# Performance work log

Measured on AMD Instinct MI355X. Metric: run time of the kernel, lower is better.

The kernel has to match this reference:

```python
import jax, jax.numpy as jnp
import numpy as np

HIDDEN = 32
SEQ = 1440
IN = 11


def lstm_layer(x, Wih, Whh, bih, bhh):
    # x: (B, T, I); PyTorch gate order i, f, g, o stacked along first dim of W (4H, I)
    B, T, _ = x.shape
    H = Whh.shape[1]
    xg = jnp.einsum('bti,gi->btg', x, Wih) + bih + bhh  # (B, T, 4H) input projections precomputed

    def step(carry, xg_t):
        h, c = carry
        g = xg_t + h @ Whh.T  # (B, 4H)
        i, f, gg, o = jnp.split(g, 4, axis=-1)
        i = jax.nn.sigmoid(i)
        f = jax.nn.sigmoid(f)
        gg = jnp.tanh(gg)
        o = jax.nn.sigmoid(o)
        c = f * c + i * gg
        h = o * jnp.tanh(c)
        return (h, c), h

    h0 = jnp.zeros((B, H), x.dtype)
    (_, _), hs = jax.lax.scan(step, (h0, h0), jnp.swapaxes(xg, 0, 1))  # hs: (T, B, H)
    return jnp.swapaxes(hs, 0, 1)


def setup_inputs() -> dict:
    key = jax.random.key(0)
    ks = jax.random.split(key, 14)
    s = 0.1
    return {
        'x': jax.random.normal(ks[0], (1024, IN, SEQ), dtype=jnp.float32),
        'Wih0': jax.random.normal(ks[1], (4 * HIDDEN, IN), dtype=jnp.float32) * s,
        'Whh0': jax.random.normal(ks[2], (4 * HIDDEN, HIDDEN), dtype=jnp.float32) * s,
        'bih0': jax.random.normal(ks[3], (4 * HIDDEN,), dtype=jnp.float32) * s,
        'bhh0': jax.random.normal(ks[4], (4 * HIDDEN,), dtype=jnp.float32) * s,
        'Wih1': jax.random.normal(ks[5], (4 * HIDDEN, HIDDEN), dtype=jnp.float32) * s,
        'Whh1': jax.random.normal(ks[6], (4 * HIDDEN, HIDDEN), dtype=jnp.float32) * s,
        'bih1': jax.random.normal(ks[7], (4 * HIDDEN,), dtype=jnp.float32) * s,
        'bhh1': jax.random.normal(ks[8], (4 * HIDDEN,), dtype=jnp.float32) * s,
        'fc1_w': jax.random.normal(ks[9], (16, HIDDEN), dtype=jnp.float32) * s,
        'fc1_b': jax.random.normal(ks[10], (16,), dtype=jnp.float32) * s,
        'fc2_w': jax.random.normal(ks[11], (1, 16), dtype=jnp.float32) * s,
        'fc2_b': jax.random.normal(ks[12], (1,), dtype=jnp.float32) * s,
    }


def reference(x, Wih0, Whh0, bih0, bhh0, Wih1, Whh1, bih1, bhh1, fc1_w, fc1_b, fc2_w, fc2_b):
    # x.view(-1, 11, 1440).transpose(1, 2) -> (B, 1440, 11)
    xt = jnp.swapaxes(x.reshape(-1, IN, SEQ), 1, 2)
    h1 = lstm_layer(xt, Wih0, Whh0, bih0, bhh0)
    h2 = lstm_layer(h1, Wih1, Whh1, bih1, bhh1)
    out = h2[:, :SEQ - 1, :]  # out[:, -1440:-1, :] with T=1440 -> steps 0..1438
    out = jnp.tanh(out @ fc1_w.T + fc1_b)
    out = out @ fc2_w.T + fc2_b
    return out.squeeze(-1)  # (B, 1439)
```

## Files before the change

### kernel.cpp

```cpp
#include <hip/hip_runtime.h>

#define H    32
#define SEQ  1440
#define NT   (SEQ - 1)
#define INP  11
#define TC   64

#define LOG2E 1.44269504f

__device__ __forceinline__ float rcp_fast(float x)  { return __builtin_amdgcn_rcpf(x); }
__device__ __forceinline__ float exp2_fast(float x) { return __builtin_amdgcn_exp2f(x); }
__device__ __forceinline__ float tanh_f(float x) {
    return fmaf(2.f, rcp_fast(1.f + exp2_fast(x * (-2.f * LOG2E))), -1.f);
}

__global__
__attribute__((amdgpu_flat_work_group_size(128, 128)))
__attribute__((amdgpu_waves_per_eu(2, 2)))
void lstm_fused_kernel(const float* __restrict__ x,
                       const float* __restrict__ Wih0, const float* __restrict__ Whh0,
                       const float* __restrict__ bih0, const float* __restrict__ bhh0,
                       const float* __restrict__ Wih1, const float* __restrict__ Whh1,
                       const float* __restrict__ bih1, const float* __restrict__ bhh1,
                       const float* __restrict__ fc1w_g, const float* __restrict__ fc1b_g,
                       const float* __restrict__ fc2w_g, const float* __restrict__ fc2b_g,
                       float* __restrict__ out)
{
    __shared__ float h0s[2][H];
    __shared__ float h1s[2][H];
    __shared__ float xs[TC][12];
    __shared__ float h1c[TC][36];

    const int tid  = threadIdx.x;
    const int lane = tid & 63;
    const int wv   = tid >> 6;
    const int m    = lane & 15;
    const int q    = lane >> 4;
    const int jj   = wv * 16 + m;
    const int r    = q * 32 + jj;
    const int b    = blockIdx.x;

    const float gsl = ((q == 2) ? 2.f : 1.f) * LOG2E;
    const float am  = (q == 2) ? 2.f : 1.f;
    const float ab  = (q == 2) ? -1.f : 0.f;

    float wx[12];
    #pragma unroll
    for (int i = 0; i < INP; ++i) wx[i] = Wih0[r * INP + i] * gsl;
    wx[11] = 0.f;
    float wh0[H], wi1[H], wh1[H];
    #pragma unroll
    for (int k = 0; k < H; ++k) {
        wh0[k] = Whh0[r * H + k] * gsl;
        wi1[k] = Wih1[r * H + k] * gsl;
        wh1[k] = Whh1[r * H + k] * gsl;
    }
    const float bs0 = (bih0[r] + bhh0[r]) * gsl;
    const float bs1 = (bih1[r] + bhh1[r]) * gsl;

    if (tid < H) { h0s[0][tid] = 0.f; h1s[0][tid] = 0.f; }
    float c0 = 0.f, c1 = 0.f;

    const float* xb   = x   + (size_t)b * INP * SEQ;
    float*       outb = out + (size_t)b * NT;

    __syncthreads();

    for (int cbase = 0; cbase < NT; cbase += TC) {
        const int clen = min(TC, NT - cbase);

        {
            const int col = tid & 63;
            const int rw  = tid >> 6;
            #pragma unroll
            for (int ib = 0; ib < 12; ib += 2) {
                const int row = ib + rw;
                if (col < clen)
                    xs[col][row] = (row < INP) ? xb[row * SEQ + cbase + col] : 0.f;
            }
        }
        __syncthreads();

        for (int tc = 0; tc < clen; ++tc) {
            const int p = (cbase + tc) & 1;

            float act;
            {
                const float4* xv = (const float4*)xs[tc];
                const float4* hv = (const float4*)h0s[p];
                float a0 = bs0, a1 = 0.f;
                float4 x0 = xv[0], x1 = xv[1], x2 = xv[2];
                a0 = fmaf(wx[0],  x0.x, a0);  a1 = fmaf(wx[1],  x0.y, a1);
                a0 = fmaf(wx[2],  x0.z, a0);  a1 = fmaf(wx[3],  x0.w, a1);
                a0 = fmaf(wx[4],  x1.x, a0);  a1 = fmaf(wx[5],  x1.y, a1);
                a0 = fmaf(wx[6],  x1.z, a0);  a1 = fmaf(wx[7],  x1.w, a1);
                a0 = fmaf(wx[8],  x2.x, a0);  a1 = fmaf(wx[9],  x2.y, a1);
                a0 = fmaf(wx[10], x2.z, a0);
                #pragma unroll
                for (int kk = 0; kk < 4; ++kk) {
                    float4 ha = hv[kk], hb = hv[kk + 4];
                    a0 = fmaf(wh0[4*kk+0],    ha.x, a0);
                    a1 = fmaf(wh0[4*kk+1],    ha.y, a1);
                    a0 = fmaf(wh0[4*kk+2],    ha.z, a0);
                    a1 = fmaf(wh0[4*kk+3],    ha.w, a1);
                    a0 = fmaf(wh0[16+4*kk+0], hb.x, a0);
                    a1 = fmaf(wh0[16+4*kk+1], hb.y, a1);
                    a0 = fmaf(wh0[16+4*kk+2], hb.z, a0);
                    a1 = fmaf(wh0[16+4*kk+3], hb.w, a1);
                }
                float a = a0 + a1;
                act = fmaf(am, rcp_fast(1.f + exp2_fast(-a)), ab);
            }
            float gf = __shfl_xor(act, 16);
            float gg = __shfl_xor(act, 32);
            float go = __shfl_xor(act, 48);
            if (q == 0) {
                c0 = fmaf(gf, c0, act * gg);
                h0s[p ^ 1][jj] = go * tanh_f(c0);
            }
            __syncthreads();

            {
                const float4* hav = (const float4*)h0s[p ^ 1];
                const float4* hbv = (const float4*)h1s[p];
                float a0 = bs1, a1 = 0.f, a2 = 0.f, a3 = 0.f;
                #pragma unroll
                for (int kk = 0; kk < 4; ++kk) {
                    float4 ha = hav[kk], ha2 = hav[kk + 4];
                    float4 hb = hbv[kk], hb2 = hbv[kk + 4];
                    a0 = fmaf(wi1[4*kk+0],    ha.x,  a0); a1 = fmaf(wi1[4*kk+1],    ha.y,  a1);
                    a2 = fmaf(wi1[4*kk+2],    ha.z,  a2); a3 = fmaf(wi1[4*kk+3],    ha.w,  a3);
                    a0 = fmaf(wi1[16+4*kk+0], ha2.x, a0); a1 = fmaf(wi1[16+4*kk+1], ha2.y, a1);
                    a2 = fmaf(wi1[16+4*kk+2], ha2.z, a2); a3 = fmaf(wi1[16+4*kk+3], ha2.w, a3);
                    a0 = fmaf(wh1[4*kk+0],    hb.x,  a0); a1 = fmaf(wh1[4*kk+1],    hb.y,  a1);
                    a2 = fmaf(wh1[4*kk+2],    hb.z,  a2); a3 = fmaf(wh1[4*kk+3],    hb.w,  a3);
                    a0 = fmaf(wh1[16+4*kk+0], hb2.x, a0); a1 = fmaf(wh1[16+4*kk+1], hb2.y, a1);
                    a2 = fmaf(wh1[16+4*kk+2], hb2.z, a2); a3 = fmaf(wh1[16+4*kk+3], hb2.w, a3);
                }
                float a = (a0 + a1) + (a2 + a3);
                act = fmaf(am, rcp_fast(1.f + exp2_fast(-a)), ab);
            }
            gf = __shfl_xor(act, 16);
            gg = __shfl_xor(act, 32);
            go = __shfl_xor(act, 48);
            if (q == 0) {
                c1 = fmaf(gf, c1, act * gg);
                float hn = go * tanh_f(c1);
                h1s[p ^ 1][jj] = hn;
                h1c[tc][jj]    = hn;
            }
            __syncthreads();
        }

        {
            const int u = tid & 15;
            float fcw[H];
            #pragma unroll
            for (int k = 0; k < H; ++k) fcw[k] = fc1w_g[u * H + k];
            const float fcb = fc1b_g[u];
            const float f2w = fc2w_g[u];
            const float f2b = fc2b_g[0];
            #pragma unroll
            for (int rep = 0; rep < 8; ++rep) {
                const int tcl = (tid >> 4) + 8 * rep;
                if (tcl < clen) {
                    const float4* hv = (const float4*)h1c[tcl];
                    float a0 = fcb, a1 = 0.f;
                    #pragma unroll
                    for (int kk = 0; kk < 4; ++kk) {
                        float4 ha = hv[kk], hb = hv[kk + 4];
                        a0 = fmaf(fcw[4*kk+0],    ha.x, a0); a1 = fmaf(fcw[4*kk+1],    ha.y, a1);
                        a0 = fmaf(fcw[4*kk+2],    ha.z, a0); a1 = fmaf(fcw[4*kk+3],    ha.w, a1);
                        a0 = fmaf(fcw[16+4*kk+0], hb.x, a0); a1 = fmaf(fcw[16+4*kk+1], hb.y, a1);
                        a0 = fmaf(fcw[16+4*kk+2], hb.z, a0); a1 = fmaf(fcw[16+4*kk+3], hb.w, a1);
                    }
                    float yv = tanh_f(a0 + a1) * f2w;
                    yv += __shfl_xor(yv, 1);
                    yv += __shfl_xor(yv, 2);
                    yv += __shfl_xor(yv, 4);
                    yv += __shfl_xor(yv, 8);
                    if (u == 0) outb[cbase + tcl] = yv + f2b;
                }
            }
        }
        __syncthreads();
    }
}

extern "C" void kernel_launch(void* const* d_in, const int* in_sizes, int n_in,
                              void* d_out, int out_size, void* d_ws, size_t ws_size,
                              hipStream_t stream)
{
    const float* x    = (const float*)d_in[0];
    const float* Wih0 = (const float*)d_in[1];
    const float* Whh0 = (const float*)d_in[2];
    const float* bih0 = (const float*)d_in[3];
    const float* bhh0 = (const float*)d_in[4];
    const float* Wih1 = (const float*)d_in[5];
    const float* Whh1 = (const float*)d_in[6];
    const float* bih1 = (const float*)d_in[7];
    const float* bhh1 = (const float*)d_in[8];
    const float* fc1w = (const float*)d_in[9];
    const float* fc1b = (const float*)d_in[10];
    const float* fc2w = (const float*)d_in[11];
    const float* fc2b = (const float*)d_in[12];
    float* out = (float*)d_out;

    const int B = in_sizes[0] / (INP * SEQ);
    dim3 grid(B), block(128);
    hipLaunchKernelGGL(lstm_fused_kernel, grid, block, 0, stream,
                       x, Wih0, Whh0, bih0, bhh0, Wih1, Whh1, bih1, bhh1,
                       fc1w, fc1b, fc2w, fc2b, out);
}
```

Measured before the change: 1.262 ms.

## Wavefront-pipeline the two LSTM layers across separate warp halves

The block grows to 256 threads. One half runs layer 0 at step p while the other half runs layer 1 at step p-1, so each time step needs one barrier instead of two and the two layers' recurrences overlap. Each half now holds only its own layer's weights, which lowers register pressure. The FC head moves into the first iteration of the next chunk, using a double-buffered h1 cache, with a final tail pass afterwards. The cost is twice as many threads per block, which may reduce how many blocks fit per CU, plus one extra pipeline step.

After: 1.522 ms. 20.6% more time.

```diff
diff --git a/kernel.cpp b/kernel.cpp
--- a/kernel.cpp
+++ b/kernel.cpp
@@ -3,6 +3,7 @@
 #define H    32
 #define SEQ  1440
 #define NT   (SEQ - 1)
+#define NPH  SEQ
 #define INP  11
 #define TC   64
 
@@ -15,8 +16,8 @@
 }
 
 __global__
-__attribute__((amdgpu_flat_work_group_size(128, 128)))
-__attribute__((amdgpu_waves_per_eu(2, 2)))
+__attribute__((amdgpu_flat_work_group_size(256, 256)))
+__attribute__((amdgpu_waves_per_eu(2, 4)))
 void lstm_fused_kernel(const float* __restrict__ x,
                        const float* __restrict__ Wih0, const float* __restrict__ Whh0,
                        const float* __restrict__ bih0, const float* __restrict__ bhh0,
@@ -29,13 +30,15 @@
     __shared__ float h0s[2][H];
     __shared__ float h1s[2][H];
     __shared__ float xs[TC][12];
-    __shared__ float h1c[TC][36];
+    __shared__ float h1c[2][TC][36];
 
     const int tid  = threadIdx.x;
-    const int lane = tid & 63;
-    const int wv   = tid >> 6;
-    const int m    = lane & 15;
-    const int q    = lane >> 4;
+    const int half = tid >> 7;
+    const int ht   = tid & 127;
+    const int l    = ht & 63;
+    const int wv   = ht >> 6;
+    const int m    = l & 15;
+    const int q    = l >> 4;
     const int jj   = wv * 16 + m;
     const int r    = q * 32 + jj;
     const int b    = blockIdx.x;
@@ -44,146 +47,185 @@
     const float am  = (q == 2) ? 2.f : 1.f;
     const float ab  = (q == 2) ? -1.f : 0.f;
 
-    float wx[12];
-    #pragma unroll
-    for (int i = 0; i < INP; ++i) wx[i] = Wih0[r * INP + i] * gsl;
-    wx[11] = 0.f;
-    float wh0[H], wi1[H], wh1[H];
-    #pragma unroll
-    for (int k = 0; k < H; ++k) {
-        wh0[k] = Whh0[r * H + k] * gsl;
-        wi1[k] = Wih1[r * H + k] * gsl;
-        wh1[k] = Whh1[r * H + k] * gsl;
+    float wA[H], wB[H], bs;
+    if (half == 0) {
+        #pragma unroll
+        for (int k = 0; k < H; ++k) wA[k] = Whh0[r * H + k] * gsl;
+        #pragma unroll
+        for (int i = 0; i < INP; ++i) wB[i] = Wih0[r * INP + i] * gsl;
+        bs = (bih0[r] + bhh0[r]) * gsl;
+    } else {
+        #pragma unroll
+        for (int k = 0; k < H; ++k) {
+            wA[k] = Wih1[r * H + k] * gsl;
+            wB[k] = Whh1[r * H + k] * gsl;
+        }
+        bs = (bih1[r] + bhh1[r]) * gsl;
     }
-    const float bs0 = (bih0[r] + bhh0[r]) * gsl;
-    const float bs1 = (bih1[r] + bhh1[r]) * gsl;
-
-    if (tid < H) { h0s[0][tid] = 0.f; h1s[0][tid] = 0.f; }
-    float c0 = 0.f, c1 = 0.f;
+
+    if (tid < H)          h0s[0][tid] = 0.f;
+    else if (tid < 2 * H) h1s[0][tid - H] = 0.f;
+    float c = 0.f;
 
     const float* xb   = x   + (size_t)b * INP * SEQ;
     float*       outb = out + (size_t)b * NT;
 
-    __syncthreads();
-
-    for (int cbase = 0; cbase < NT; cbase += TC) {
-        const int clen = min(TC, NT - cbase);
+    for (int cb = 0; cb < NPH; cb += TC) {
+        const int plen = min(TC, NPH - cb);
 
         {
             const int col = tid & 63;
             const int rw  = tid >> 6;
-            #pragma unroll
-            for (int ib = 0; ib < 12; ib += 2) {
-                const int row = ib + rw;
-                if (col < clen)
-                    xs[col][row] = (row < INP) ? xb[row * SEQ + cbase + col] : 0.f;
+            if (col < plen) {
+                #pragma unroll
+                for (int ib = 0; ib < 3; ++ib) {
+                    const int row = ib * 4 + rw;
+                    xs[col][row] = (row < INP) ? xb[row * SEQ + cb + col] : 0.f;
+                }
             }
         }
         __syncthreads();
 
-        for (int tc = 0; tc < clen; ++tc) {
-            const int p = (cbase + tc) & 1;
-
-            float act;
-            {
-                const float4* xv = (const float4*)xs[tc];
-                const float4* hv = (const float4*)h0s[p];
-                float a0 = bs0, a1 = 0.f;
-                float4 x0 = xv[0], x1 = xv[1], x2 = xv[2];
-                a0 = fmaf(wx[0],  x0.x, a0);  a1 = fmaf(wx[1],  x0.y, a1);
-                a0 = fmaf(wx[2],  x0.z, a0);  a1 = fmaf(wx[3],  x0.w, a1);
-                a0 = fmaf(wx[4],  x1.x, a0);  a1 = fmaf(wx[5],  x1.y, a1);
-                a0 = fmaf(wx[6],  x1.z, a0);  a1 = fmaf(wx[7],  x1.w, a1);
-                a0 = fmaf(wx[8],  x2.x, a0);  a1 = fmaf(wx[9],  x2.y, a1);
-                a0 = fmaf(wx[10], x2.z, a0);
-                #pragma unroll
-                for (int kk = 0; kk < 4; ++kk) {
-                    float4 ha = hv[kk], hb = hv[kk + 4];
-                    a0 = fmaf(wh0[4*kk+0],    ha.x, a0);
-                    a1 = fmaf(wh0[4*kk+1],    ha.y, a1);
-                    a0 = fmaf(wh0[4*kk+2],    ha.z, a0);
-                    a1 = fmaf(wh0[4*kk+3],    ha.w, a1);
-                    a0 = fmaf(wh0[16+4*kk+0], hb.x, a0);
-                    a1 = fmaf(wh0[16+4*kk+1], hb.y, a1);
-                    a0 = fmaf(wh0[16+4*kk+2], hb.z, a0);
-                    a1 = fmaf(wh0[16+4*kk+3], hb.w, a1);
-                }
-                float a = a0 + a1;
-                act = fmaf(am, rcp_fast(1.f + exp2_fast(-a)), ab);
-            }
-            float gf = __shfl_xor(act, 16);
-            float gg = __shfl_xor(act, 32);
-            float go = __shfl_xor(act, 48);
-            if (q == 0) {
-                c0 = fmaf(gf, c0, act * gg);
-                h0s[p ^ 1][jj] = go * tanh_f(c0);
-            }
-            __syncthreads();
-
-            {
-                const float4* hav = (const float4*)h0s[p ^ 1];
-                const float4* hbv = (const float4*)h1s[p];
-                float a0 = bs1, a1 = 0.f, a2 = 0.f, a3 = 0.f;
-                #pragma unroll
-                for (int kk = 0; kk < 4; ++kk) {
-                    float4 ha = hav[kk], ha2 = hav[kk + 4];
-                    float4 hb = hbv[kk], hb2 = hbv[kk + 4];
-                    a0 = fmaf(wi1[4*kk+0],    ha.x,  a0); a1 = fmaf(wi1[4*kk+1],    ha.y,  a1);
-                    a2 = fmaf(wi1[4*kk+2],    ha.z,  a2); a3 = fmaf(wi1[4*kk+3],    ha.w,  a3);
-                    a0 = fmaf(wi1[16+4*kk+0], ha2.x, a0); a1 = fmaf(wi1[16+4*kk+1], ha2.y, a1);
-                    a2 = fmaf(wi1[16+4*kk+2], ha2.z, a2); a3 = fmaf(wi1[16+4*kk+3], ha2.w, a3);
-                    a0 = fmaf(wh1[4*kk+0],    hb.x,  a0); a1 = fmaf(wh1[4*kk+1],    hb.y,  a1);
-                    a2 = fmaf(wh1[4*kk+2],    hb.z,  a2); a3 = fmaf(wh1[4*kk+3],    hb.w,  a3);
-                    a0 = fmaf(wh1[16+4*kk+0], hb2.x, a0); a1 = fmaf(wh1[16+4*kk+1], hb2.y, a1);
-                    a2 = fmaf(wh1[16+4*kk+2], hb2.z, a2); a3 = fmaf(wh1[16+4*kk+3], hb2.w, a3);
-                }
-                float a = (a0 + a1) + (a2 + a3);
-                act = fmaf(am, rcp_fast(1.f + exp2_fast(-a)), ab);
-            }
-            gf = __shfl_xor(act, 16);
-            gg = __shfl_xor(act, 32);
-            go = __shfl_xor(act, 48);
-            if (q == 0) {
-                c1 = fmaf(gf, c1, act * gg);
-                float hn = go * tanh_f(c1);
-                h1s[p ^ 1][jj] = hn;
-                h1c[tc][jj]    = hn;
-            }
-            __syncthreads();
-        }
-
-        {
-            const int u = tid & 15;
-            float fcw[H];
-            #pragma unroll
-            for (int k = 0; k < H; ++k) fcw[k] = fc1w_g[u * H + k];
-            const float fcb = fc1b_g[u];
-            const float f2w = fc2w_g[u];
-            const float f2b = fc2b_g[0];
-            #pragma unroll
-            for (int rep = 0; rep < 8; ++rep) {
-                const int tcl = (tid >> 4) + 8 * rep;
-                if (tcl < clen) {
-                    const float4* hv = (const float4*)h1c[tcl];
-                    float a0 = fcb, a1 = 0.f;
+        for (int pc = 0; pc < plen; ++pc) {
+            const int p = cb + pc;
+            if (half == 0) {
+                if (p < NT) {
+                    const float4* xv = (const float4*)xs[pc];
+                    const float4* hv = (const float4*)h0s[p & 1];
+                    float a0 = bs, a1 = 0.f;
+                    float4 x0 = xv[0], x1 = xv[1], x2 = xv[2];
+                    a0 = fmaf(wB[0],  x0.x, a0);  a1 = fmaf(wB[1],  x0.y, a1);
+                    a0 = fmaf(wB[2],  x0.z, a0);  a1 = fmaf(wB[3],  x0.w, a1);
+                    a0 = fmaf(wB[4],  x1.x, a0);  a1 = fmaf(wB[5],  x1.y, a1);
+                    a0 = fmaf(wB[6],  x1.z, a0);  a1 = fmaf(wB[7],  x1.w, a1);
+                    a0 = fmaf(wB[8],  x2.x, a0);  a1 = fmaf(wB[9],  x2.y, a1);
+                    a0 = fmaf(wB[10], x2.z, a0);
                     #pragma unroll
                     for (int kk = 0; kk < 4; ++kk) {
                         float4 ha = hv[kk], hb = hv[kk + 4];
-                        a0 = fmaf(fcw[4*kk+0],    ha.x, a0); a1 = fmaf(fcw[4*kk+1],    ha.y, a1);
-                        a0 = fmaf(fcw[4*kk+2],    ha.z, a0); a1 = fmaf(fcw[4*kk+3],    ha.w, a1);
-                        a0 = fmaf(fcw[16+4*kk+0], hb.x, a0); a1 = fmaf(fcw[16+4*kk+1], hb.y, a1);
-                        a0 = fmaf(fcw[16+4*kk+2], hb.z, a0); a1 = fmaf(fcw[16+4*kk+3], hb.w, a1);
-                    }
-                    float yv = tanh_f(a0 + a1) * f2w;
-                    yv += __shfl_xor(yv, 1);
-                    yv += __shfl_xor(yv, 2);
-                    yv += __shfl_xor(yv, 4);
-                    yv += __shfl_xor(yv, 8);
-                    if (u == 0) outb[cbase + tcl] = yv + f2b;
-                }
-            }
-        }
-        __syncthreads();
+                        a0 = fmaf(wA[4*kk+0],    ha.x, a0);
+                        a1 = fmaf(wA[4*kk+1],    ha.y, a1);
+                        a0 = fmaf(wA[4*kk+2],    ha.z, a0);
+                        a1 = fmaf(wA[4*kk+3],    ha.w, a1);
+                        a0 = fmaf(wA[16+4*kk+0], hb.x, a0);
+                        a1 = fmaf(wA[16+4*kk+1], hb.y, a1);
+                        a0 = fmaf(wA[16+4*kk+2], hb.z, a0);
+                        a1 = fmaf(wA[16+4*kk+3], hb.w, a1);
+                    }
+                    float a   = a0 + a1;
+                    float act = fmaf(am, rcp_fast(1.f + exp2_fast(-a)), ab);
+                    float gf = __shfl_xor(act, 16);
+                    float gg = __shfl_xor(act, 32);
+                    float go = __shfl_xor(act, 48);
+                    if (q == 0) {
+                        c = fmaf(gf, c, act * gg);
+                        h0s[(p & 1) ^ 1][jj] = go * tanh_f(c);
+                    }
+                }
+            } else {
+                if (p >= 1) {
+                    const int s = p - 1;
+                    const float4* iv = (const float4*)h0s[p & 1];
+                    const float4* hv = (const float4*)h1s[s & 1];
+                    float a0 = bs, a1 = 0.f, a2 = 0.f, a3 = 0.f;
+                    #pragma unroll
+                    for (int kk = 0; kk < 4; ++kk) {
+                        float4 ia = iv[kk], ia2 = iv[kk + 4];
+                        float4 ha = hv[kk], ha2 = hv[kk + 4];
+                        a0 = fmaf(wA[4*kk+0],    ia.x,  a0); a1 = fmaf(wA[4*kk+1],    ia.y,  a1);
+                        a2 = fmaf(wA[4*kk+2],    ia.z,  a2); a3 = fmaf(wA[4*kk+3],    ia.w,  a3);
+                        a0 = fmaf(wA[16+4*kk+0], ia2.x, a0); a1 = fmaf(wA[16+4*kk+1], ia2.y, a1);
+                        a2 = fmaf(wA[16+4*kk+2], ia2.z, a2); a3 = fmaf(wA[16+4*kk+3], ia2.w, a3);
+                        a0 = fmaf(wB[4*kk+0],    ha.x,  a0); a1 = fmaf(wB[4*kk+1],    ha.y,  a1);
+                        a2 = fmaf(wB[4*kk+2],    ha.z,  a2); a3 = fmaf(wB[4*kk+3],    ha.w,  a3);
+                        a0 = fmaf(wB[16+4*kk+0], ha2.x, a0); a1 = fmaf(wB[16+4*kk+1], ha2.y, a1);
+                        a2 = fmaf(wB[16+4*kk+2], ha2.z, a2); a3 = fmaf(wB[16+4*kk+3], ha2.w, a3);
+                    }
+                    float a   = (a0 + a1) + (a2 + a3);
+                    float act = fmaf(am, rcp_fast(1.f + exp2_fast(-a)), ab);
+                    float gf = __shfl_xor(act, 16);
+                    float gg = __shfl_xor(act, 32);
+                    float go = __shfl_xor(act, 48);
+                    if (q == 0) {
+                        c = fmaf(gf, c, act * gg);
+                        float hn = go * tanh_f(c);
+                        h1s[(s & 1) ^ 1][jj] = hn;
+                        h1c[(s >> 6) & 1][s & 63][jj] = hn;
+                    }
+                }
+            }
+            __syncthreads();
+
+            if (pc == 0 && cb >= TC) {
+                const float (*hc)[36] = h1c[((cb >> 6) - 1) & 1];
+                const int u  = tid & 15;
+                const int kh = (tid >> 4) & 1;
+                const int sl = tid >> 5;
+                float fw[16];
+                #pragma unroll
+                for (int k = 0; k < 16; ++k) fw[k] = fc1w_g[u * H + kh * 16 + k];
+                const float fb = fc1b_g[u], f2w = fc2w_g[u], f2b = fc2b_g[0];
+                float* outc = outb + (cb - TC);
+                #pragma unroll
+                for (int rep = 0; rep < 8; ++rep) {
+                    const int t2 = sl + 8 * rep;
+                    const float4* hv = (const float4*)&hc[t2][kh * 16];
+                    float a0 = 0.f, a1 = 0.f;
+                    float4 v0 = hv[0], v1 = hv[1], v2 = hv[2], v3 = hv[3];
+                    a0 = fmaf(fw[0],  v0.x, a0);  a1 = fmaf(fw[1],  v0.y, a1);
+                    a0 = fmaf(fw[2],  v0.z, a0);  a1 = fmaf(fw[3],  v0.w, a1);
+                    a0 = fmaf(fw[4],  v1.x, a0);  a1 = fmaf(fw[5],  v1.y, a1);
+                    a0 = fmaf(fw[6],  v1.z, a0);  a1 = fmaf(fw[7],  v1.w, a1);
+                    a0 = fmaf(fw[8],  v2.x, a0);  a1 = fmaf(fw[9],  v2.y, a1);
+                    a0 = fmaf(fw[10], v2.z, a0);  a1 = fmaf(fw[11], v2.w, a1);
+                    a0 = fmaf(fw[12], v3.x, a0);  a1 = fmaf(fw[13], v3.y, a1);
+                    a0 = fmaf(fw[14], v3.z, a0);  a1 = fmaf(fw[15], v3.w, a1);
+                    float y = a0 + a1;
+                    y += __shfl_xor(y, 16);
+                    float z = tanh_f(y + fb) * f2w;
+                    z += __shfl_xor(z, 1);  z += __shfl_xor(z, 2);
+                    z += __shfl_xor(z, 4);  z += __shfl_xor(z, 8);
+                    if ((tid & 31) == 0) outc[t2] = z + f2b;
+                }
+            }
+        }
+    }
+
+    {
+        const int tbase = ((NPH - 1) / TC) * TC;
+        const int tlen  = NT - tbase;
+        const float (*hc)[36] = h1c[(tbase >> 6) & 1];
+        const int u  = tid & 15;
+        const int kh = (tid >> 4) & 1;
+        const int sl = tid >> 5;
+        float fw[16];
+        #pragma unroll
+        for (int k = 0; k < 16; ++k) fw[k] = fc1w_g[u * H + kh * 16 + k];
+        const float fb = fc1b_g[u], f2w = fc2w_g[u], f2b = fc2b_g[0];
+        float* outc = outb + tbase;
+        #pragma unroll
+        for (int rep = 0; rep < 8; ++rep) {
+            const int t2 = sl + 8 * rep;
+            if (t2 < tlen) {
+                const float4* hv = (const float4*)&hc[t2][kh * 16];
+                float a0 = 0.f, a1 = 0.f;
+                float4 v0 = hv[0], v1 = hv[1], v2 = hv[2], v3 = hv[3];
+                a0 = fmaf(fw[0],  v0.x, a0);  a1 = fmaf(fw[1],  v0.y, a1);
+                a0 = fmaf(fw[2],  v0.z, a0);  a1 = fmaf(fw[3],  v0.w, a1);
+                a0 = fmaf(fw[4],  v1.x, a0);  a1 = fmaf(fw[5],  v1.y, a1);
+                a0 = fmaf(fw[6],  v1.z, a0);  a1 = fmaf(fw[7],  v1.w, a1);
+                a0 = fmaf(fw[8],  v2.x, a0);  a1 = fmaf(fw[9],  v2.y, a1);
+                a0 = fmaf(fw[10], v2.z, a0);  a1 = fmaf(fw[11], v2.w, a1);
+                a0 = fmaf(fw[12], v3.x, a0);  a1 = fmaf(fw[13], v3.y, a1);
+                a0 = fmaf(fw[14], v3.z, a0);  a1 = fmaf(fw[15], v3.w, a1);
+                float y = a0 + a1;
+                y += __shfl_xor(y, 16);
+                float z = tanh_f(y + fb) * f2w;
+                z += __shfl_xor(z, 1);  z += __shfl_xor(z, 2);
+                z += __shfl_xor(z, 4);  z += __shfl_xor(z, 8);
+                if ((tid & 31) == 0) outc[t2] = z + f2b;
+            }
+        }
     }
 }
 
@@ -207,7 +249,7 @@
     float* out = (float*)d_out;
 
     const int B = in_sizes[0] / (INP * SEQ);
-    dim3 grid(B), block(128);
+    dim3 grid(B), block(256);
     hipLaunchKernelGGL(lstm_fused_kernel, grid, block, 0, stream,
                        x, Wih0, Whh0, bih0, bhh0, Wih1, Whh1, bih1, bhh1,
                        fc1w, fc1b, fc2w, fc2b, out);
```

## Process two sequences per block with split-K gate dot products across 256 threads

Applied to the files above, without the earlier changes.

Each block now handles two batch elements with 256 threads. Each gate row's dot product is split across two half-waves (kh) and the halves are combined with a cross-lane shuffle. Per-thread weight registers are halved, and the per-timestep barrier cost is spread over two sequences. A large padding LDS array is added, apparently to limit how many blocks fit on a CU. The price is an extra shuffle per gate, twice the serial gate work per step inside one block, and half as many blocks in the grid.

Measured after the change: 1.943 ms. +54.0%, slower.

```diff
diff --git a/kernel.cpp b/kernel.cpp
--- a/kernel.cpp
+++ b/kernel.cpp
@@ -15,7 +15,7 @@
 }
 
 __global__
-__attribute__((amdgpu_flat_work_group_size(128, 128)))
+__attribute__((amdgpu_flat_work_group_size(256, 256)))
 __attribute__((amdgpu_waves_per_eu(2, 2)))
 void lstm_fused_kernel(const float* __restrict__ x,
                        const float* __restrict__ Wih0, const float* __restrict__ Whh0,
@@ -26,43 +26,50 @@
                        const float* __restrict__ fc2w_g, const float* __restrict__ fc2b_g,
                        float* __restrict__ out)
 {
-    __shared__ float h0s[2][H];
-    __shared__ float h1s[2][H];
-    __shared__ float xs[TC][12];
-    __shared__ float h1c[TC][36];
-
-    const int tid  = threadIdx.x;
-    const int lane = tid & 63;
-    const int wv   = tid >> 6;
-    const int m    = lane & 15;
-    const int q    = lane >> 4;
-    const int jj   = wv * 16 + m;
-    const int r    = q * 32 + jj;
-    const int b    = blockIdx.x;
+    __shared__ float h0s[2][2][H];
+    __shared__ float h1s[2][2][H];
+    __shared__ float xs[2][TC][12];
+    __shared__ float h1c[2][TC][36];
+    __shared__ float ldspad[10240];
+
+    const int tid = threadIdx.x;
+    ((volatile float*)ldspad)[tid] = 0.f;
+
+    const int l   = tid & 63;
+    const int wv  = tid >> 6;
+    const int m   = l & 7;
+    const int q   = (l >> 3) & 3;
+    const int kh  = l >> 5;
+    const int jj  = wv * 8 + m;
+    const int r   = q * 32 + jj;
+    const int b   = blockIdx.x;
 
     const float gsl = ((q == 2) ? 2.f : 1.f) * LOG2E;
     const float am  = (q == 2) ? 2.f : 1.f;
     const float ab  = (q == 2) ? -1.f : 0.f;
 
-    float wx[12];
+    float wh0[16], wi1[16], wh1[16], wx[6];
     #pragma unroll
-    for (int i = 0; i < INP; ++i) wx[i] = Wih0[r * INP + i] * gsl;
-    wx[11] = 0.f;
-    float wh0[H], wi1[H], wh1[H];
+    for (int k = 0; k < 16; ++k) {
+        wh0[k] = Whh0[r * H + kh * 16 + k] * gsl;
+        wi1[k] = Wih1[r * H + kh * 16 + k] * gsl;
+        wh1[k] = Whh1[r * H + kh * 16 + k] * gsl;
+    }
     #pragma unroll
-    for (int k = 0; k < H; ++k) {
-        wh0[k] = Whh0[r * H + k] * gsl;
-        wi1[k] = Wih1[r * H + k] * gsl;
-        wh1[k] = Whh1[r * H + k] * gsl;
+    for (int i = 0; i < 6; ++i) {
+        const int gi = kh * 6 + i;
+        wx[i] = (gi < INP) ? Wih0[r * INP + gi] * gsl : 0.f;
     }
-    const float bs0 = (bih0[r] + bhh0[r]) * gsl;
-    const float bs1 = (bih1[r] + bhh1[r]) * gsl;
-
-    if (tid < H) { h0s[0][tid] = 0.f; h1s[0][tid] = 0.f; }
-    float c0 = 0.f, c1 = 0.f;
-
-    const float* xb   = x   + (size_t)b * INP * SEQ;
-    float*       outb = out + (size_t)b * NT;
+    const float bs0 = (kh == 0) ? (bih0[r] + bhh0[r]) * gsl : 0.f;
+    const float bs1 = (kh == 0) ? (bih1[r] + bhh1[r]) * gsl : 0.f;
+
+    if (tid < 2 * H)          h0s[0][tid >> 5][tid & 31] = 0.f;
+    else if (tid < 4 * H)     h1s[0][(tid >> 5) & 1][tid & 31] = 0.f;
+    float c0[2] = {0.f, 0.f}, c1[2] = {0.f, 0.f};
+
+    const float* xb0  = x + ((size_t)(2 * b) + 0) * INP * SEQ;
+    const float* xb1  = x + ((size_t)(2 * b) + 1) * INP * SEQ;
+    float*       outb = out + (size_t)(2 * b) * NT;
 
     __syncthreads();
 
@@ -72,11 +79,13 @@
         {
             const int col = tid & 63;
             const int rw  = tid >> 6;
-            #pragma unroll
-            for (int ib = 0; ib < 12; ib += 2) {
-                const int row = ib + rw;
-                if (col < clen)
-                    xs[col][row] = (row < INP) ? xb[row * SEQ + cbase + col] : 0.f;
+            if (col < clen) {
+                #pragma unroll
+                for (int ib = 0; ib < 3; ++ib) {
+                    const int row = ib * 4 + rw;
+                    xs[0][col][row] = (row < INP) ? xb0[row * SEQ + cbase + col] : 0.f;
+                    xs[1][col][row] = (row < INP) ? xb1[row * SEQ + cbase + col] : 0.f;
+                }
             }
         }
         __syncthreads();
@@ -84,87 +93,92 @@
         for (int tc = 0; tc < clen; ++tc) {
             const int p = (cbase + tc) & 1;
 
-            float act;
-            {
-                const float4* xv = (const float4*)xs[tc];
-                const float4* hv = (const float4*)h0s[p];
+            #pragma unroll
+            for (int s = 0; s < 2; ++s) {
+                const float2* xv = (const float2*)&xs[s][tc][kh * 6];
+                const float4* hv = (const float4*)&h0s[p][s][kh * 16];
                 float a0 = bs0, a1 = 0.f;
-                float4 x0 = xv[0], x1 = xv[1], x2 = xv[2];
-                a0 = fmaf(wx[0],  x0.x, a0);  a1 = fmaf(wx[1],  x0.y, a1);
-                a0 = fmaf(wx[2],  x0.z, a0);  a1 = fmaf(wx[3],  x0.w, a1);
-                a0 = fmaf(wx[4],  x1.x, a0);  a1 = fmaf(wx[5],  x1.y, a1);
-                a0 = fmaf(wx[6],  x1.z, a0);  a1 = fmaf(wx[7],  x1.w, a1);
-                a0 = fmaf(wx[8],  x2.x, a0);  a1 = fmaf(wx[9],  x2.y, a1);
-                a0 = fmaf(wx[10], x2.z, a0);
-                #pragma unroll
-                for (int kk = 0; kk < 4; ++kk) {
-                    float4 ha = hv[kk], hb = hv[kk + 4];
-                    a0 = fmaf(wh0[4*kk+0],    ha.x, a0);
-                    a1 = fmaf(wh0[4*kk+1],    ha.y, a1);
-                    a0 = fmaf(wh0[4*kk+2],    ha.z, a0);
-                    a1 = fmaf(wh0[4*kk+3],    ha.w, a1);
-                    a0 = fmaf(wh0[16+4*kk+0], hb.x, a0);
-                    a1 = fmaf(wh0[16+4*kk+1], hb.y, a1);
-                    a0 = fmaf(wh0[16+4*kk+2], hb.z, a0);
-                    a1 = fmaf(wh0[16+4*kk+3], hb.w, a1);
-                }
+                float2 x0 = xv[0], x1 = xv[1], x2 = xv[2];
+                a0 = fmaf(wx[0], x0.x, a0);  a1 = fmaf(wx[1], x0.y, a1);
+                a0 = fmaf(wx[2], x1.x, a0);  a1 = fmaf(wx[3], x1.y, a1);
+                a0 = fmaf(wx[4], x2.x, a0);  a1 = fmaf(wx[5], x2.y, a1);
+                float4 h0 = hv[0], h1v = hv[1], h2v = hv[2], h3v = hv[3];
+                a0 = fmaf(wh0[0],  h0.x,  a0);  a1 = fmaf(wh0[1],  h0.y,  a1);
+                a0 = fmaf(wh0[2],  h0.z,  a0);  a1 = fmaf(wh0[3],  h0.w,  a1);
+                a0 = fmaf(wh0[4],  h1v.x, a0);  a1 = fmaf(wh0[5],  h1v.y, a1);
+                a0 = fmaf(wh0[6],  h1v.z, a0);  a1 = fmaf(wh0[7],  h1v.w, a1);
+                a0 = fmaf(wh0[8],  h2v.x, a0);  a1 = fmaf(wh0[9],  h2v.y, a1);
+                a0 = fmaf(wh0[10], h2v.z, a0);  a1 = fmaf(wh0[11], h2v.w, a1);
+                a0 = fmaf(wh0[12], h3v.x, a0);  a1 = fmaf(wh0[13], h3v.y, a1);
+                a0 = fmaf(wh0[14], h3v.z, a0);  a1 = fmaf(wh0[15], h3v.w, a1);
                 float a = a0 + a1;
-                act = fmaf(am, rcp_fast(1.f + exp2_fast(-a)), ab);
-            }
-            float gf = __shfl_xor(act, 16);
-            float gg = __shfl_xor(act, 32);
-            float go = __shfl_xor(act, 48);
-            if (q == 0) {
-                c0 = fmaf(gf, c0, act * gg);
-                h0s[p ^ 1][jj] = go * tanh_f(c0);
+                a += __shfl_xor(a, 32);
+                float act = fmaf(am, rcp_fast(1.f + exp2_fast(-a)), ab);
+                float gf = __shfl_xor(act, 8);
+                float gg = __shfl_xor(act, 16);
+                float go = __shfl_xor(act, 24);
+                if ((l & 56) == 0) {
+                    c0[s] = fmaf(gf, c0[s], act * gg);
+                    h0s[p ^ 1][s][jj] = go * tanh_f(c0[s]);
+                }
             }
             __syncthreads();
 
-            {
-                const float4* hav = (const float4*)h0s[p ^ 1];
-                const float4* hbv = (const float4*)h1s[p];
+            #pragma unroll
+            for (int s = 0; s < 2; ++s) {
+                const float4* iv = (const float4*)&h0s[p ^ 1][s][kh * 16];
+                const float4* hv = (const float4*)&h1s[p][s][kh * 16];
                 float a0 = bs1, a1 = 0.f, a2 = 0.f, a3 = 0.f;
-                #pragma unroll
-                for (int kk = 0; kk < 4; ++kk) {
-                    float4 ha = hav[kk], ha2 = hav[kk + 4];
-                    float4 hb = hbv[kk], hb2 = hbv[kk + 4];
-                    a0 = fmaf(wi1[4*kk+0],    ha.x,  a0); a1 = fmaf(wi1[4*kk+1],    ha.y,  a1);
-                    a2 = fmaf(wi1[4*kk+2],    ha.z,  a2); a3 = fmaf(wi1[4*kk+3],    ha.w,  a3);
-                    a0 = fmaf(wi1[16+4*kk+0], ha2.x, a0); a1 = fmaf(wi1[16+4*kk+1], ha2.y, a1);
-                    a2 = fmaf(wi1[16+4*kk+2], ha2.z, a2); a3 = fmaf(wi1[16+4*kk+3], ha2.w, a3);
-                    a0 = fmaf(wh1[4*kk+0],    hb.x,  a0); a1 = fmaf(wh1[4*kk+1],    hb.y,  a1);
-                    a2 = fmaf(wh1[4*kk+2],    hb.z,  a2); a3 = fmaf(wh1[4*kk+3],    hb.w,  a3);
-                    a0 = fmaf(wh1[16+4*kk+0], hb2.x, a0); a1 = fmaf(wh1[16+4*kk+1], hb2.y, a1);
-                    a2 = fmaf(wh1[16+4*kk+2], hb2.z, a2); a3 = fmaf(wh1[16+4*kk+3], hb2.w, a3);
-                }
+                float4 i0 = iv[0], i1 = iv[1], i2 = iv[2], i3 = iv[3];
+                float4 g0 = hv[0], g1 = hv[1], g2 = hv[2], g3 = hv[3];
+                a0 = fmaf(wi1[0],  i0.x, a0);  a1 = fmaf(wi1[1],  i0.y, a1);
+                a2 = fmaf(wi1[2],  i0.z, a2);  a3 = fmaf(wi1[3],  i0.w, a3);
+                a0 = fmaf(wi1[4],  i1.x, a0);  a1 = fmaf(wi1[5],  i1.y, a1);
+                a2 = fmaf(wi1[6],  i1.z, a2);  a3 = fmaf(wi1[7],  i1.w, a3);
+                a0 = fmaf(wi1[8],  i2.x, a0);  a1 = fmaf(wi1[9],  i2.y, a1);
+                a2 = fmaf(wi1[10], i2.z, a2);  a3 = fmaf(wi1[11], i2.w, a3);
+                a0 = fmaf(wi1[12], i3.x, a0);  a1 = fmaf(wi1[13], i3.y, a1);
+                a2 = fmaf(wi1[14], i3.z, a2);  a3 = fmaf(wi1[15], i3.w, a3);
+                a0 = fmaf(wh1[0],  g0.x, a0);  a1 = fmaf(wh1[1],  g0.y, a1);
+                a2 = fmaf(wh1[2],  g0.z, a2);  a3 = fmaf(wh1[3],  g0.w, a3);
+                a0 = fmaf(wh1[4],  g1.x, a0);  a1 = fmaf(wh1[5],  g1.y, a1);
+                a2 = fmaf(wh1[6],  g1.z, a2);  a3 = fmaf(wh1[7],  g1.w, a3);
+                a0 = fmaf(wh1[8],  g2.x, a0);  a1 = fmaf(wh1[9],  g2.y, a1);
+                a2 = fmaf(wh1[10], g2.z, a2);  a3 = fmaf(wh1[11], g2.w, a3);
+                a0 = fmaf(wh1[12], g3.x, a0);  a1 = fmaf(wh1[13], g3.y, a1);
+                a2 = fmaf(wh1[14], g3.z, a2);  a3 = fmaf(wh1[15], g3.w, a3);
                 float a = (a0 + a1) + (a2 + a3);
-                act = fmaf(am, rcp_fast(1.f + exp2_fast(-a)), ab);
-            }
-            gf = __shfl_xor(act, 16);
-            gg = __shfl_xor(act, 32);
-            go = __shfl_xor(act, 48);
-            if (q == 0) {
-                c1 = fmaf(gf, c1, act * gg);
-                float hn = go * tanh_f(c1);
-                h1s[p ^ 1][jj] = hn;
-                h1c[tc][jj]    = hn;
+                a += __shfl_xor(a, 32);
+                float act = fmaf(am, rcp_fast(1.f + exp2_fast(-a)), ab);
+                float gf = __shfl_xor(act, 8);
+                float gg = __shfl_xor(act, 16);
+                float go = __shfl_xor(act, 24);
+                if ((l & 56) == 0) {
+                    c1[s] = fmaf(gf, c1[s], act * gg);
+                    float hn = go * tanh_f(c1[s]);
+                    h1s[p ^ 1][s][jj] = hn;
+                    h1c[s][tc][jj]    = hn;
+                }
             }
             __syncthreads();
         }
 
         {
-            const int u = tid & 15;
+            const int sfc = tid >> 7;
+            const int ht  = tid & 127;
+            const int u   = ht & 15;
             float fcw[H];
             #pragma unroll
             for (int k = 0; k < H; ++k) fcw[k] = fc1w_g[u * H + k];
             const float fcb = fc1b_g[u];
             const float f2w = fc2w_g[u];
             const float f2b = fc2b_g[0];
+            float* outc = outb + (size_t)sfc * NT + cbase;
             #pragma unroll
             for (int rep = 0; rep < 8; ++rep) {
-                const int tcl = (tid >> 4) + 8 * rep;
+                const int tcl = (ht >> 4) + 8 * rep;
                 if (tcl < clen) {
-                    const float4* hv = (const float4*)h1c[tcl];
+                    const float4* hv = (const float4*)h1c[sfc][tcl];
                     float a0 = fcb, a1 = 0.f;
                     #pragma unroll
                     for (int kk = 0; kk < 4; ++kk) {
@@ -179,7 +193,7 @@
                     yv += __shfl_xor(yv, 2);
                     yv += __shfl_xor(yv, 4);
                     yv += __shfl_xor(yv, 8);
-                    if (u == 0) outb[cbase + tcl] = yv + f2b;
+                    if (u == 0) outc[tcl] = yv + f2b;
                 }
             }
         }
@@ -207,7 +221,7 @@
     float* out = (float*)d_out;
 
     const int B = in_sizes[0] / (INP * SEQ);
-    dim3 grid(B), block(128);
+    dim3 grid(B / 2), block(256);
     hipLaunchKernelGGL(lstm_fused_kernel, grid, block, 0, stream,
                        x, Wih0, Whh0, bih0, bhh0, Wih1, Whh1, bih1, bhh1,
                        fc1w, fc1b, fc2w, fc2b, out);
```
